# Optimization experiments

Hardware: AMD Instinct MI355X
Metric: run time of the kernel (lower is better)

The kernel has to match this reference:

```python
import jax, jax.numpy as jnp
import numpy as np

N, E, G = 50000, 200000, 1000
EPS = 1e-5
NEG_SLOPE = 0.2


def setup_inputs() -> dict:
    key = jax.random.key(0)
    ks = jax.random.split(key, 24)
    p = lambda k, shape: jax.random.normal(k, shape, jnp.float32) * 0.05
    inp = {
        "x": jax.random.normal(ks[0], (N, 64), jnp.float32),
        "edge_index": jax.random.randint(ks[1], (2, E), 0, N, jnp.int32),
        "batch": jnp.sort(jax.random.randint(ks[2], (N,), 0, G, jnp.int32)),
        "solvent_fingerprint": jax.random.uniform(ks[3], (G, 128), jnp.float32),
        # GAT layer 1: 64 -> 4 heads x 128
        "W1": p(ks[4], (64, 512)), "a1_src": p(ks[5], (4, 128)), "a1_dst": p(ks[6], (4, 128)), "b1": jnp.zeros((512,), jnp.float32),
        "bn1_g": jnp.ones((512,), jnp.float32), "bn1_b": jnp.zeros((512,), jnp.float32),
        # GAT layer 2: 512 -> 4 heads x 256
        "W2": p(ks[7], (512, 1024)), "a2_src": p(ks[8], (4, 256)), "a2_dst": p(ks[9], (4, 256)), "b2": jnp.zeros((1024,), jnp.float32),
        "bn2_g": jnp.ones((1024,), jnp.float32), "bn2_b": jnp.zeros((1024,), jnp.float32),
        # GCN: 1024 -> 256
        "Wg": p(ks[10], (1024, 256)), "bg": jnp.zeros((256,), jnp.float32),
        "bn3_g": jnp.ones((256,), jnp.float32), "bn3_b": jnp.zeros((256,), jnp.float32),
        # MLP head
        "Ws": p(ks[11], (128, 128)), "bs": jnp.zeros((128,), jnp.float32),
        "Wf1": p(ks[12], (640, 128)), "bf1": jnp.zeros((128,), jnp.float32),
        "bnf_g": jnp.ones((128,), jnp.float32), "bnf_b": jnp.zeros((128,), jnp.float32),
        "Wf2": p(ks[13], (128, 1)), "bf2": jnp.zeros((1,), jnp.float32),
    }
    return inp


def _batchnorm(x, g, b):
    mu = x.mean(0)
    var = x.var(0)
    return (x - mu) * jax.lax.rsqrt(var + EPS) * g + b


def _gat(x, src, dst, W, a_src, a_dst, b, H, C):
    n = x.shape[0]
    h = (x @ W).reshape(n, H, C)                      # [N,H,C]
    al_s = (h * a_src).sum(-1)                        # [N,H]
    al_d = (h * a_dst).sum(-1)                        # [N,H]
    e = jax.nn.leaky_relu(al_s[src] + al_d[dst], NEG_SLOPE)   # [E,H]
    m = jax.ops.segment_max(e, dst, num_segments=n)
    ex = jnp.exp(e - m[dst])
    s = jax.ops.segment_sum(ex, dst, num_segments=n)
    alpha = ex / jnp.maximum(s[dst], 1e-16)
    out = jax.ops.segment_sum(h[src] * alpha[..., None], dst, num_segments=n)  # [N,H,C]
    return out.reshape(n, H * C) + b


def _gcn(x, src, dst, W, b):
    n = x.shape[0]
    h = x @ W
    deg = jax.ops.segment_sum(jnp.ones_like(dst, jnp.float32), dst, num_segments=n)
    dinv = jax.lax.rsqrt(jnp.maximum(deg, 1.0))
    norm = dinv[src] * dinv[dst]
    return jax.ops.segment_sum(h[src] * norm[:, None], dst, num_segments=n) + b


def reference(x, edge_index, batch, solvent_fingerprint,
              W1, a1_src, a1_dst, b1, bn1_g, bn1_b,
              W2, a2_src, a2_dst, b2, bn2_g, bn2_b,
              Wg, bg, bn3_g, bn3_b,
              Ws, bs, Wf1, bf1, bnf_g, bnf_b, Wf2, bf2):
    n = x.shape[0]
    loops = jnp.arange(n, dtype=edge_index.dtype)
    src = jnp.concatenate([edge_index[0], loops])
    dst = jnp.concatenate([edge_index[1], loops])

    h = _gat(x, src, dst, W1, a1_src, a1_dst, b1, 4, 128)
    h = jax.nn.relu(_batchnorm(h, bn1_g, bn1_b))
    h = _gat(h, src, dst, W2, a2_src, a2_dst, b2, 4, 256)
    h = jax.nn.relu(_batchnorm(h, bn2_g, bn2_b))
    h = _gcn(h, src, dst, Wg, bg)
    h = jax.nn.relu(_batchnorm(h, bn3_g, bn3_b))

    cnt = jax.ops.segment_sum(jnp.ones((n,), jnp.float32), batch, num_segments=G)
    gap = jax.ops.segment_sum(h, batch, num_segments=G) / jnp.maximum(cnt, 1.0)[:, None]
    gmp = jax.ops.segment_max(h, batch, num_segments=G)
    gmp = jnp.where(jnp.isfinite(gmp), gmp, 0.0)

    solv = jax.nn.relu(solvent_fingerprint @ Ws + bs)
    z = jnp.concatenate([gap, gmp, solv], axis=1)          # [G,640]
    z = jax.nn.relu(_batchnorm(z @ Wf1 + bf1, bnf_g, bnf_b))
    # dropout: identity in eval/deterministic reference
    return jax.nn.sigmoid(z @ Wf2 + bf2)
```

## Files before the change

kernel.cpp:

```cpp
#include <hip/hip_runtime.h>
#include <cmath>

#define LEAK 0.2f
#define BN_EPS 1e-5f

static inline int cdiv(long long a, long long b){ return (int)((a + b - 1) / b); }

typedef __attribute__((ext_vector_type(8))) short bf16x8;
typedef __attribute__((ext_vector_type(4))) float f32x4;

__device__ __forceinline__ float bf2f(unsigned short u){
    return __uint_as_float(((unsigned int)u) << 16);
}
__device__ __forceinline__ unsigned short f2bf(float f){
    unsigned int u = __float_as_uint(f);
    u += 0x7FFFu + ((u >> 16) & 1u);
    return (unsigned short)(u >> 16);
}
__device__ __forceinline__ float edge_ex(float s, float d){
    float t = s + d;
    t = (t >= 0.f) ? t : LEAK * t;
    return __expf(t);
}

#define GLOAD_LDS16(gsrc, ldst) \
    __builtin_amdgcn_global_load_lds( \
        (const __attribute__((address_space(1))) unsigned int*)(gsrc), \
        (__attribute__((address_space(3))) unsigned int*)(ldst), 16, 0, 0)

__global__ __launch_bounds__(256) void gemm_mfma(
    const unsigned short* __restrict__ A, const unsigned short* __restrict__ Bt,
    unsigned short* __restrict__ D, int M, int K, int lda, int ldb, int ldc,
    int NX, int NYT)
{
    const int id = blockIdx.x;
    const int xcd = id & 7;
    const int j = id >> 3;
    const int bx = j % NX;
    const int by = (j / NX) * 8 + xcd;
    if (by >= NYT) return;

    __shared__ unsigned short As[128 * 64];
    __shared__ unsigned short Bs[128 * 64];
    const int t = threadIdx.x;
    const int row0 = by * 128, col0 = bx * 128;
    const int lane = t & 63, wv = t >> 6;
    const int wm = (wv >> 1) << 6, wn = (wv & 1) << 6;
    const int lm = lane & 15, lq = lane >> 4;

    const int sr  = t >> 3;
    const int scs = (t & 7) << 3;
    const int gsw = (((t & 7) ^ (sr & 7)) << 3);
    const unsigned short* ap[4];
    const unsigned short* bp[4];
    unsigned short* la[4];
    unsigned short* lb[4];
    #pragma unroll
    for (int q = 0; q < 4; ++q) {
        int r = sr + q * 32;
        int gra = row0 + r; if (gra >= M) gra = M - 1;
        ap[q] = A  + (size_t)gra * lda + gsw;
        bp[q] = Bt + (size_t)(col0 + r) * ldb + gsw;
        la[q] = &As[r * 64 + scs];
        lb[q] = &Bs[r * 64 + scs];
    }

    f32x4 acc[4][4] = {};
    const int rx = lm & 7;

    for (int k0 = 0; k0 < K; k0 += 64) {
        #pragma unroll
        for (int q = 0; q < 4; ++q) {
            GLOAD_LDS16(ap[q] + k0, la[q]);
            GLOAD_LDS16(bp[q] + k0, lb[q]);
        }
        __syncthreads();

        #pragma unroll
        for (int kk = 0; kk < 2; ++kk) {
            const int ck = (((kk << 2) + lq) ^ rx) << 3;
            bf16x8 af[4], bfr[4];
            #pragma unroll
            for (int mi = 0; mi < 4; ++mi)
                af[mi] = *(const bf16x8*)&As[(wm + mi * 16 + lm) * 64 + ck];
            #pragma unroll
            for (int ni = 0; ni < 4; ++ni)
                bfr[ni] = *(const bf16x8*)&Bs[(wn + ni * 16 + lm) * 64 + ck];
            #pragma unroll
            for (int mi = 0; mi < 4; ++mi)
                #pragma unroll
                for (int ni = 0; ni < 4; ++ni)
                    acc[mi][ni] = __builtin_amdgcn_mfma_f32_16x16x32_bf16(
                        af[mi], bfr[ni], acc[mi][ni], 0, 0, 0);
        }
        __syncthreads();
    }

    #pragma unroll
    for (int mi = 0; mi < 4; ++mi) {
        int row_b = row0 + wm + mi * 16 + lq * 4;
        #pragma unroll
        for (int ni = 0; ni < 4; ++ni) {
            int col = col0 + wn + ni * 16 + lm;
            #pragma unroll
            for (int r = 0; r < 4; ++r) {
                int row = row_b + r;
                if (row < M) D[(size_t)row * ldc + col] = f2bf(acc[mi][ni][r]);
            }
        }
    }
}

__global__ __launch_bounds__(256) void logits_valu(
    const unsigned short* __restrict__ A, const unsigned short* __restrict__ vat,
    float* __restrict__ C, int M, int K)
{
    __shared__ unsigned short vs[8 * 512];
    const int t = threadIdx.x;
    for (int i = t; i < K; i += 256)
        *(bf16x8*)&vs[i * 8] = *(const bf16x8*)(vat + (size_t)i * 8);
    __syncthreads();

    const int lane = t & 63;
    const int w = blockIdx.x * 4 + (t >> 6);
    const int Gl = K >> 3;
    const int rpw = 64 / Gl;
    const int sub = lane / Gl;
    const int li = lane - sub * Gl;
    long long row = (long long)w * rpw + sub;
    if (row >= M) return;

    bf16x8 hv = *(const bf16x8*)(A + row * K + li * 8);
    float hf[8];
    #pragma unroll
    for (int j = 0; j < 8; ++j) hf[j] = bf2f((unsigned short)hv[j]);

    float s[8];
    #pragma unroll
    for (int o = 0; o < 8; ++o) {
        bf16x8 v = *(const bf16x8*)&vs[o * K + li * 8];
        float acc = 0.f;
        #pragma unroll
        for (int j = 0; j < 8; ++j) acc += hf[j] * bf2f((unsigned short)v[j]);
        s[o] = acc;
    }
    for (int off = Gl >> 1; off; off >>= 1) {
        #pragma unroll
        for (int o = 0; o < 8; ++o) s[o] += __shfl_xor(s[o], off);
    }
    #pragma unroll
    for (int o = 0; o < 8; ++o)
        if (li == o) C[row * 8 + o] = s[o];
}

__global__ __launch_bounds__(256) void prep_all(
    const float* __restrict__ W1, const float* __restrict__ W2,
    const float* __restrict__ Wg, const float* __restrict__ x,
    const float* __restrict__ a1s, const float* __restrict__ a1d,
    const float* __restrict__ a2s, const float* __restrict__ a2d,
    const int* __restrict__ batch,
    unsigned short* __restrict__ W1bdt, unsigned short* __restrict__ W2t,
    unsigned short* __restrict__ Wgt, unsigned short* __restrict__ xb,
    unsigned short* __restrict__ vat1, unsigned short* __restrict__ vat2,
    int* __restrict__ cursor, int* __restrict__ gptr,
    int N, int G_,
    int c0, int c1, int c2, int c3, int c4, int c5, int c6)
{
    const int t = threadIdx.x;
    const int bid = blockIdx.x;
    if (bid < c0) {
        int i = bid * 256 + t;
        int o = i >> 8, k = i & 255;
        unsigned short v = 0;
        if ((k >> 6) == (o >> 7)) v = f2bf(W1[(size_t)(k & 63) * 512 + o]);
        W1bdt[i] = v;
    } else if (bid < c1) {
        int i = (bid - c0) * 256 + t;
        int k = i >> 10, n = i & 1023;
        W2t[(size_t)n * 512 + k] = f2bf(W2[i]);
    } else if (bid < c2) {
        int i = (bid - c1) * 256 + t;
        int k = i >> 8, n = i & 255;
        Wgt[(size_t)n * 1024 + k] = f2bf(Wg[i]);
    } else if (bid < c3) {
        int i = (bid - c2) * 256 + t;
        if (i < N * 16) {
            float4 v = *reinterpret_cast<const float4*>(x + (size_t)i * 4);
            ushort4 o = { f2bf(v.x), f2bf(v.y), f2bf(v.z), f2bf(v.w) };
            *reinterpret_cast<ushort4*>(xb + (size_t)i * 4) = o;
        }
    } else if (bid < c4) {
        int w = (((bid - c3) * 256 + t) >> 6);
        int lane = t & 63;
        int k = w >> 2, h = w & 3;
        const float* wp = W1 + (size_t)k * 512 + h * 128;
        const float* as = a1s + h * 128;
        const float* ad = a1d + h * 128;
        float s = 0.f, d = 0.f;
        for (int c = lane; c < 128; c += 64) {
            float v = wp[c];
            s += v * as[c];
            d += v * ad[c];
        }
        #pragma unroll
        for (int off = 32; off; off >>= 1) {
            s += __shfl_down(s, off);
            d += __shfl_down(d, off);
        }
        if (lane == 0) {
            vat1[(size_t)h * 64 + k] = f2bf(s);
            vat1[(size_t)(4 + h) * 64 + k] = f2bf(d);
        }
    } else if (bid < c5) {
        int w = (((bid - c4) * 256 + t) >> 6);
        int lane = t & 63;
        int k = w >> 2, h = w & 3;
        const float* wp = W2 + (size_t)k * 1024 + h * 256;
        const float* as = a2s + h * 256;
        const float* ad = a2d + h * 256;
        float s = 0.f, d = 0.f;
        for (int c = lane; c < 256; c += 64) {
            float v = wp[c];
            s += v * as[c];
            d += v * ad[c];
        }
        #pragma unroll
        for (int off = 32; off; off >>= 1) {
            s += __shfl_down(s, off);
            d += __shfl_down(d, off);
        }
        if (lane == 0) {
            vat2[(size_t)h * 512 + k] = f2bf(s);
            vat2[(size_t)(4 + h) * 512 + k] = f2bf(d);
        }
    } else if (bid < c6) {
        int i = (bid - c5) * 256 + t;
        if (i < N) cursor[i] = 1;
    } else {
        int g = (bid - c6) * 256 + t;
        if (g > G_) return;
        if (g == G_) { gptr[G_] = N; return; }
        int lo = 0, hi = N;
        while (lo < hi) { int mid = (lo + hi) >> 1; if (batch[mid] < g) lo = mid + 1; else hi = mid; }
        gptr[g] = lo;
    }
}

template<bool RELU>
__global__ __launch_bounds__(256) void gemm_small(
    const float* __restrict__ A, const float* __restrict__ B,
    const float* __restrict__ bias, float* __restrict__ C,
    int M, int K, int lda, int ldb, int ldc)
{
    __shared__ float As[2][640];
    const int t = threadIdx.x;
    const int r = t >> 7, c = t & 127;
    const int row0 = blockIdx.x * 2;
    for (int i = t; i < 2 * K; i += 256) {
        int rr = i / K, kk = i - rr * K;
        int gr = row0 + rr;
        As[rr][kk] = (gr < M) ? A[(size_t)gr * lda + kk] : 0.f;
    }
    __syncthreads();
    float acc0 = 0.f, acc1 = 0.f;
    for (int k = 0; k < K; k += 8) {
        float4 a0 = *reinterpret_cast<const float4*>(&As[r][k]);
        float4 a1 = *reinterpret_cast<const float4*>(&As[r][k + 4]);
        acc0 += a0.x * B[(size_t)(k + 0) * ldb + c];
        acc1 += a0.y * B[(size_t)(k + 1) * ldb + c];
        acc0 += a0.z * B[(size_t)(k + 2) * ldb + c];
        acc1 += a0.w * B[(size_t)(k + 3) * ldb + c];
        acc0 += a1.x * B[(size_t)(k + 4) * ldb + c];
        acc1 += a1.y * B[(size_t)(k + 5) * ldb + c];
        acc0 += a1.z * B[(size_t)(k + 6) * ldb + c];
        acc1 += a1.w * B[(size_t)(k + 7) * ldb + c];
    }
    int row = row0 + r;
    if (row < M) {
        float v = acc0 + acc1;
        if (bias) v += bias[c];
        if (RELU) v = fmaxf(v, 0.f);
        C[(size_t)row * ldc + c] = v;
    }
}

__device__ __forceinline__ int e_src(const int* es, int E, int k){ return k < E ? es[k] : k - E; }
__device__ __forceinline__ int e_dst(const int* ed, int E, int k){ return k < E ? ed[k] : k - E; }

__global__ void hist_dst(const int* __restrict__ ed, int E, int* __restrict__ cnt)
{
    int k = blockIdx.x * blockDim.x + threadIdx.x;
    if (k < E) atomicAdd(&cnt[ed[k]], 1);
}

__global__ __launch_bounds__(256) void scan_blk(const int* __restrict__ cnt,
                                                int* __restrict__ rowptr,
                                                int* __restrict__ bsums, int n)
{
    __shared__ int ts[256];
    const int t = threadIdx.x;
    const int i0 = blockIdx.x * 1024 + t * 4;
    int4 v = {0, 0, 0, 0};
    if (i0 + 3 < n) v = *reinterpret_cast<const int4*>(cnt + i0);
    else {
        if (i0 + 0 < n) v.x = cnt[i0 + 0];
        if (i0 + 1 < n) v.y = cnt[i0 + 1];
        if (i0 + 2 < n) v.z = cnt[i0 + 2];
        if (i0 + 3 < n) v.w = cnt[i0 + 3];
    }
    int lsum = v.x + v.y + v.z + v.w;
    ts[t] = lsum;
    __syncthreads();
    #pragma unroll
    for (int off = 1; off < 256; off <<= 1) {
        int u = (t >= off) ? ts[t - off] : 0;
        __syncthreads();
        ts[t] += u;
        __syncthreads();
    }
    int excl = ts[t] - lsum;
    if (i0 + 0 < n) rowptr[i0 + 0] = excl;
    if (i0 + 1 < n) rowptr[i0 + 1] = excl + v.x;
    if (i0 + 2 < n) rowptr[i0 + 2] = excl + v.x + v.y;
    if (i0 + 3 < n) rowptr[i0 + 3] = excl + v.x + v.y + v.z;
    if (t == 255) bsums[blockIdx.x] = ts[255];
}

__global__ __launch_bounds__(256) void scan_tops(int* __restrict__ bsums,
                                                 int* __restrict__ rowptr, int nb, int n)
{
    __shared__ int ts[256];
    const int t = threadIdx.x;
    int v = (t < nb) ? bsums[t] : 0;
    ts[t] = v;
    __syncthreads();
    #pragma unroll
    for (int off = 1; off < 256; off <<= 1) {
        int u = (t >= off) ? ts[t - off] : 0;
        __syncthreads();
        ts[t] += u;
        __syncthreads();
    }
    if (t < nb) bsums[t] = ts[t] - v;
    if (t == 255) rowptr[n] = ts[255];
}

__global__ void scan_add(int* __restrict__ rowptr, int* __restrict__ cursor,
                         const int* __restrict__ bsums, int n)
{
    int i = blockIdx.x * blockDim.x + threadIdx.x;
    if (i >= n) return;
    int r = rowptr[i] + bsums[i >> 10];
    rowptr[i] = r;
    cursor[i] = r;
}

__global__ void csr_scatter_dinv(const int* __restrict__ es, const int* __restrict__ ed,
                                 int E, int Etot, int* __restrict__ cursor,
                                 int* __restrict__ col,
                                 const int* __restrict__ rowptr,
                                 float* __restrict__ dinv, int N, int NBsc)
{
    const int bid = blockIdx.x;
    const int t = threadIdx.x;
    if (bid < NBsc) {
        int k = bid * 256 + t;
        if (k >= Etot) return;
        int sn = e_src(es, E, k), dn = e_dst(ed, E, k);
        int pos = atomicAdd(&cursor[dn], 1);
        col[pos] = sn;
    } else {
        int i = (bid - NBsc) * 256 + t;
        if (i < N) dinv[i] = rsqrtf(fmaxf((float)(rowptr[i + 1] - rowptr[i]), 1.f));
    }
}

__global__ void gat_agg4_64(const int* __restrict__ rowptr, const int* __restrict__ col,
                            const unsigned short* __restrict__ xb,
                            const float* __restrict__ alsd,
                            unsigned short* __restrict__ agg, int N)
{
    int w = (int)(((long long)blockIdx.x * blockDim.x + threadIdx.x) >> 6);
    int lane = threadIdx.x & 63;
    if (w >= N) return;
    float4 dt = *reinterpret_cast<const float4*>(alsd + (size_t)w * 8 + 4);
    int r0 = rowptr[w], r1 = rowptr[w + 1];
    float a0 = 0.f, a1 = 0.f, a2 = 0.f, a3 = 0.f;
    float s0 = 0.f, s1 = 0.f, s2 = 0.f, s3 = 0.f;
    for (int e = r0; e < r1; ++e) {
        int sn = col[e];
        float4 st = *reinterpret_cast<const float4*>(alsd + (size_t)sn * 8);
        float e0 = edge_ex(st.x, dt.x);
        float e1 = edge_ex(st.y, dt.y);
        float e2 = edge_ex(st.z, dt.z);
        float e3 = edge_ex(st.w, dt.w);
        float xA = bf2f(xb[(size_t)sn * 64 + lane]);
        a0 += e0 * xA; s0 += e0;
        a1 += e1 * xA; s1 += e1;
        a2 += e2 * xA; s2 += e2;
        a3 += e3 * xA; s3 += e3;
    }
    unsigned short* op = agg + (size_t)w * 256 + lane;
    op[0]   = f2bf(a0 / fmaxf(s0, 1e-16f));
    op[64]  = f2bf(a1 / fmaxf(s1, 1e-16f));
    op[128] = f2bf(a2 / fmaxf(s2, 1e-16f));
    op[192] = f2bf(a3 / fmaxf(s3, 1e-16f));
}

__global__ void gat_gather512_ex(const int* __restrict__ rowptr, const int* __restrict__ col,
                                 const unsigned short* __restrict__ h, int ldh,
                                 const float* __restrict__ alsd, int pr,
                                 unsigned short* __restrict__ out, int N)
{
    int w = (int)(((long long)blockIdx.x * blockDim.x + threadIdx.x) >> 6);
    int lane = threadIdx.x & 63;
    if (w >= N) return;
    float2 dt = *reinterpret_cast<const float2*>(alsd + (size_t)w * 8 + 4 + 2 * pr);
    int r0 = rowptr[w], r1 = rowptr[w + 1];
    float s0 = 0.f, s1 = 0.f;
    float a00=0.f,a01=0.f,a02=0.f,a03=0.f;
    float a10=0.f,a11=0.f,a12=0.f,a13=0.f;
    for (int e = r0; e < r1; ++e) {
        int sn = col[e];
        float2 st = *reinterpret_cast<const float2*>(alsd + (size_t)sn * 8 + 2 * pr);
        float e0 = edge_ex(st.x, dt.x);
        float e1 = edge_ex(st.y, dt.y);
        const unsigned short* p = h + (size_t)sn * ldh + lane * 4;
        ushort4 h0 = *reinterpret_cast<const ushort4*>(p);
        ushort4 h1 = *reinterpret_cast<const ushort4*>(p + 256);
        s0 += e0; s1 += e1;
        a00 += bf2f(h0.x) * e0; a01 += bf2f(h0.y) * e0;
        a02 += bf2f(h0.z) * e0; a03 += bf2f(h0.w) * e0;
        a10 += bf2f(h1.x) * e1; a11 += bf2f(h1.y) * e1;
        a12 += bf2f(h1.z) * e1; a13 += bf2f(h1.w) * e1;
    }
    float i0 = 1.f / fmaxf(s0, 1e-16f);
    float i1 = 1.f / fmaxf(s1, 1e-16f);
    ushort4 o0 = { f2bf(a00*i0), f2bf(a01*i0), f2bf(a02*i0), f2bf(a03*i0) };
    ushort4 o1 = { f2bf(a10*i1), f2bf(a11*i1), f2bf(a12*i1), f2bf(a13*i1) };
    unsigned short* op = out + (size_t)w * 512 + lane * 4;
    *reinterpret_cast<ushort4*>(op)       = o0;
    *reinterpret_cast<ushort4*>(op + 256) = o1;
}

__global__ void gcn_gather256(const int* __restrict__ rowptr, const int* __restrict__ col,
                              const unsigned short* __restrict__ h,
                              const float* __restrict__ dinv,
                              unsigned short* __restrict__ out, int N)
{
    int w = (int)(((long long)blockIdx.x * blockDim.x + threadIdx.x) >> 6);
    int lane = threadIdx.x & 63;
    if (w >= N) return;
    int r0 = rowptr[w], r1 = rowptr[w + 1];
    float a0 = 0.f, a1 = 0.f, a2 = 0.f, a3 = 0.f;
    int e = r0;
    for (; e + 1 < r1; e += 2) {
        int sn0 = col[e], sn1 = col[e + 1];
        float w0 = dinv[sn0], w1 = dinv[sn1];
        ushort4 hv0 = *reinterpret_cast<const ushort4*>(h + (size_t)sn0 * 256 + lane * 4);
        ushort4 hv1 = *reinterpret_cast<const ushort4*>(h + (size_t)sn1 * 256 + lane * 4);
        a0 += bf2f(hv0.x) * w0 + bf2f(hv1.x) * w1;
        a1 += bf2f(hv0.y) * w0 + bf2f(hv1.y) * w1;
        a2 += bf2f(hv0.z) * w0 + bf2f(hv1.z) * w1;
        a3 += bf2f(hv0.w) * w0 + bf2f(hv1.w) * w1;
    }
    if (e < r1) {
        int sn = col[e];
        float wv = dinv[sn];
        ushort4 hv = *reinterpret_cast<const ushort4*>(h + (size_t)sn * 256 + lane * 4);
        a0 += bf2f(hv.x) * wv; a1 += bf2f(hv.y) * wv;
        a2 += bf2f(hv.z) * wv; a3 += bf2f(hv.w) * wv;
    }
    float dn = dinv[w];
    ushort4 o;
    o.x = f2bf(a0 * dn); o.y = f2bf(a1 * dn);
    o.z = f2bf(a2 * dn); o.w = f2bf(a3 * dn);
    *reinterpret_cast<ushort4*>(out + (size_t)w * 256 + lane * 4) = o;
}

template<int D>
__global__ __launch_bounds__(256) void bn_part(
    const float* __restrict__ x, float* __restrict__ ps, float* __restrict__ pq,
    int M, int Y)
{
    constexpr int DG = D / 4;
    constexpr int P  = 256 / DG;
    const int t = threadIdx.x;
    const int cg = t % DG, ph = t / DG;
    const int y = blockIdx.y;
    const int rows_per = (M + Y - 1) / Y;
    const int r0 = y * rows_per;
    const int r1 = min(r0 + rows_per, M);
    float s0=0,s1=0,s2=0,s3=0,q0=0,q1=0,q2=0,q3=0;
    for (int r = r0 + ph; r < r1; r += P) {
        float4 v = *reinterpret_cast<const float4*>(x + (size_t)r * D + cg * 4);
        s0+=v.x; s1+=v.y; s2+=v.z; s3+=v.w;
        q0+=v.x*v.x; q1+=v.y*v.y; q2+=v.z*v.z; q3+=v.w*v.w;
    }
    __shared__ float ls[P][D];
    __shared__ float lq[P][D];
    ls[ph][cg*4+0]=s0; ls[ph][cg*4+1]=s1; ls[ph][cg*4+2]=s2; ls[ph][cg*4+3]=s3;
    lq[ph][cg*4+0]=q0; lq[ph][cg*4+1]=q1; lq[ph][cg*4+2]=q2; lq[ph][cg*4+3]=q3;
    __syncthreads();
    if (ph == 0) {
        #pragma unroll
        for (int j = 0; j < 4; ++j) {
            float ss = 0.f, qq = 0.f;
            #pragma unroll
            for (int p = 0; p < P; ++p) { ss += ls[p][cg*4+j]; qq += lq[p][cg*4+j]; }
            ps[(size_t)y * D + cg*4 + j] = ss;
            pq[(size_t)y * D + cg*4 + j] = qq;
        }
    }
}

template<int D>
__global__ __launch_bounds__(256) void bn_part_bf(
    const unsigned short* __restrict__ x, int ldx,
    float* __restrict__ ps, float* __restrict__ pq, int M, int Y)
{
    constexpr int DG = D / 4;
    constexpr int P  = 256 / DG;
    const int t = threadIdx.x;
    const int cg = t % DG, ph = t / DG;
    const int y = blockIdx.y;
    const int rows_per = (M + Y - 1) / Y;
    const int r0 = y * rows_per;
    const int r1 = min(r0 + rows_per, M);
    float s0=0,s1=0,s2=0,s3=0,q0=0,q1=0,q2=0,q3=0;
    for (int r = r0 + ph; r < r1; r += P) {
        ushort4 u = *reinterpret_cast<const ushort4*>(x + (size_t)r * ldx + cg * 4);
        float vx = bf2f(u.x), vy = bf2f(u.y), vz = bf2f(u.z), vw = bf2f(u.w);
        s0+=vx; s1+=vy; s2+=vz; s3+=vw;
        q0+=vx*vx; q1+=vy*vy; q2+=vz*vz; q3+=vw*vw;
    }
    __shared__ float ls[P][D];
    __shared__ float lq[P][D];
    ls[ph][cg*4+0]=s0; ls[ph][cg*4+1]=s1; ls[ph][cg*4+2]=s2; ls[ph][cg*4+3]=s3;
    lq[ph][cg*4+0]=q0; lq[ph][cg*4+1]=q1; lq[ph][cg*4+2]=q2; lq[ph][cg*4+3]=q3;
    __syncthreads();
    if (ph == 0) {
        #pragma unroll
        for (int j = 0; j < 4; ++j) {
            float ss = 0.f, qq = 0.f;
            #pragma unroll
            for (int p = 0; p < P; ++p) { ss += ls[p][cg*4+j]; qq += lq[p][cg*4+j]; }
            ps[(size_t)y * D + cg*4 + j] = ss;
            pq[(size_t)y * D + cg*4 + j] = qq;
        }
    }
}

template<int D>
__global__ __launch_bounds__(256) void bn_reduce_fin(
    const float* __restrict__ ps, const float* __restrict__ pq,
    const float* __restrict__ g, const float* __restrict__ b,
    float* __restrict__ scale, float* __restrict__ shift, int Y, float invM)
{
    const int t = threadIdx.x;
    const int cl = t & 63;
    const int c = blockIdx.x * 64 + cl;
    const int ph = t >> 6;
    float s = 0.f, q = 0.f;
    for (int y = ph; y < Y; y += 4) {
        s += ps[(size_t)y * D + c];
        q += pq[(size_t)y * D + c];
    }
    __shared__ float ls[4][64];
    __shared__ float lq[4][64];
    ls[ph][cl] = s; lq[ph][cl] = q;
    __syncthreads();
    if (ph == 0) {
        s = ls[0][cl] + ls[1][cl] + ls[2][cl] + ls[3][cl];
        q = lq[0][cl] + lq[1][cl] + lq[2][cl] + lq[3][cl];
        float mu = s * invM;
        float var = q * invM - mu * mu;
        float rs = rsqrtf(var + BN_EPS) * g[c];
        scale[c] = rs;
        shift[c] = b[c] - mu * rs;
    }
}

__global__ void bn_apply_bfbf(const unsigned short* __restrict__ x,
                              const float* __restrict__ scale, const float* __restrict__ shift,
                              unsigned short* __restrict__ dst, int total4, int Cb4,
                              int ldx, int ldd)
{
    int i = blockIdx.x * blockDim.x + threadIdx.x;
    if (i >= total4) return;
    int r = i / Cb4, c4 = (i - r * Cb4) * 4;
    ushort4 u = *reinterpret_cast<const ushort4*>(x + (size_t)r * ldx + c4);
    float4 sc = *reinterpret_cast<const float4*>(scale + c4);
    float4 sh = *reinterpret_cast<const float4*>(shift + c4);
    ushort4 o;
    o.x = f2bf(fmaxf(bf2f(u.x) * sc.x + sh.x, 0.f));
    o.y = f2bf(fmaxf(bf2f(u.y) * sc.y + sh.y, 0.f));
    o.z = f2bf(fmaxf(bf2f(u.z) * sc.z + sh.z, 0.f));
    o.w = f2bf(fmaxf(bf2f(u.w) * sc.w + sh.w, 0.f));
    *reinterpret_cast<ushort4*>(dst + (size_t)r * ldd + c4) = o;
}

__global__ __launch_bounds__(256) void pool_gather_bn(const unsigned short* __restrict__ h,
                                                      const float* __restrict__ scale,
                                                      const float* __restrict__ shift,
                                                      const int* __restrict__ gptr,
                                                      float* __restrict__ z, int G_)
{
    int g = blockIdx.x;
    int c = threadIdx.x;
    int r0 = gptr[g], r1 = gptr[g + 1];
    float sc = scale[c], sh = shift[c];
    float s = 0.f, m = 0.f;
    int i = r0;
    for (; i + 1 < r1; i += 2) {
        float v0 = fmaxf(bf2f(h[(size_t)i * 256 + c]) * sc + sh, 0.f);
        float v1 = fmaxf(bf2f(h[(size_t)(i + 1) * 256 + c]) * sc + sh, 0.f);
        s += v0 + v1;
        m = fmaxf(m, fmaxf(v0, v1));
    }
    if (i < r1) {
        float v = fmaxf(bf2f(h[(size_t)i * 256 + c]) * sc + sh, 0.f);
        s += v;
        m = fmaxf(m, v);
    }
    float cnt = fmaxf((float)(r1 - r0), 1.f);
    z[(size_t)g * 640 + c] = s / cnt;
    z[(size_t)g * 640 + 256 + c] = m;
}

__global__ void final_head_bn(const float* __restrict__ f1,
                              const float* __restrict__ scale, const float* __restrict__ shift,
                              const float* __restrict__ Wf2, const float* __restrict__ bf2,
                              float* __restrict__ out, int G_)
{
    int w = (int)(((long long)blockIdx.x * blockDim.x + threadIdx.x) >> 6);
    int lane = threadIdx.x & 63;
    if (w >= G_) return;
    float s = 0.f;
    #pragma unroll
    for (int q = 0; q < 2; ++q) {
        int c = lane + q * 64;
        float v = fmaxf(f1[(size_t)w * 128 + c] * scale[c] + shift[c], 0.f);
        s += v * Wf2[c];
    }
    #pragma unroll
    for (int off = 32; off; off >>= 1) s += __shfl_down(s, off);
    if (lane == 0) out[w] = 1.f / (1.f + __expf(-(s + bf2[0])));
}

__global__ void sentinel(float* __restrict__ out, int n, float v)
{
    int i = blockIdx.x * blockDim.x + threadIdx.x;
    if (i < n) out[i] = v;
}

extern "C" void kernel_launch(void* const* d_in, const int* in_sizes, int n_in,
                              void* d_out, int out_size, void* d_ws, size_t ws_size,
                              hipStream_t stream)
{
    const float* x    = (const float*)d_in[0];
    const int*   ei   = (const int*)d_in[1];
    const int*   batch= (const int*)d_in[2];
    const float* sfp  = (const float*)d_in[3];
    const float* W1   = (const float*)d_in[4];
    const float* a1s  = (const float*)d_in[5];
    const float* a1d  = (const float*)d_in[6];
    const float* bn1g = (const float*)d_in[8];
    const float* bn1b = (const float*)d_in[9];
    const float* W2   = (const float*)d_in[10];
    const float* a2s  = (const float*)d_in[11];
    const float* a2d  = (const float*)d_in[12];
    const float* bn2g = (const float*)d_in[14];
    const float* bn2b = (const float*)d_in[15];
    const float* Wg   = (const float*)d_in[16];
    const float* bn3g = (const float*)d_in[18];
    const float* bn3b = (const float*)d_in[19];
    const float* Wsm  = (const float*)d_in[20];
    const float* bsm  = (const float*)d_in[21];
    const float* Wf1  = (const float*)d_in[22];
    const float* bnfg = (const float*)d_in[24];
    const float* bnfb = (const float*)d_in[25];
    const float* Wf2  = (const float*)d_in[26];
    const float* bf2  = (const float*)d_in[27];
    float* outp = (float*)d_out;

    const int N    = in_sizes[0] / 64;
    const int E    = in_sizes[1] / 2;
    const int G_   = in_sizes[3] / 128;
    const int Etot = E + N;
    const int* esrc = ei;
    const int* edst = ei + E;
    const int YB = 256;
    const int NB = cdiv(N, 1024);
    const int NYT = cdiv(N, 128);
    const int NYT8 = cdiv(NYT, 8) * 8;

    float* ws = (float*)d_ws;
    size_t off = 0;
    float* accA  = ws + off; off += (size_t)N * 256;
    float* h3acc = ws + off; off += (size_t)N * 256;
    unsigned short* g1b   = (unsigned short*)accA;
    unsigned short* g3b   = (unsigned short*)accA;
    unsigned short* h2all = (unsigned short*)accA;
    unsigned short* R1 = (unsigned short*)(ws + off); off += (size_t)N * 256;
    unsigned short* o1n = R1;
    unsigned short* hb  = (unsigned short*)(ws + off); off += (size_t)N * 128;
    unsigned short* xb  = (unsigned short*)(ws + off); off += (size_t)N * 32;
    float* alsd = ws + off; off += (size_t)N * 8;
    float* dinv = ws + off; off += N;
    float* bsc = ws + off; off += 1024;
    float* bsh = ws + off; off += 1024;
    float* ps  = ws + off; off += (size_t)YB * 512;
    float* pq  = ws + off; off += (size_t)YB * 512;
    float* z   = ws + off; off += (size_t)G_ * 640;
    float* f1  = ws + off; off += (size_t)G_ * 128;
    int* rowptr = (int*)(ws + off); off += (size_t)(N + 1);
    int* colc   = (int*)(ws + off); off += (size_t)Etot;
    int* gptr   = (int*)(ws + off); off += (size_t)(G_ + 1);
    int* bsums  = (int*)(ws + off); off += 256;
    off = (off + 3) & ~(size_t)3;
    unsigned short* vat1 = (unsigned short*)(ws + off); off += 128 * 64 / 2;
    unsigned short* vat2 = (unsigned short*)(ws + off); off += 128 * 512 / 2;
    unsigned short* W1bdt = (unsigned short*)(ws + off); off += 512 * 256 / 2;
    unsigned short* W2t = (unsigned short*)(ws + off); off += 512 * 1024 / 2;
    unsigned short* Wgt = (unsigned short*)(ws + off); off += 1024 * 256 / 2;
    int* cursor = (int*)alsd;
    size_t need = off * 4;
    if (ws_size < need) {
        sentinel<<<cdiv(out_size, 256), 256, 0, stream>>>(outp, out_size, (float)(ws_size >> 20));
        return;
    }

    const int BLK = 256;
    dim3 blk(BLK);

    const int c0 = 512;
    const int c1 = c0 + 2048;
    const int c2 = c1 + 1024;
    const int c3 = c2 + cdiv((long long)N * 16, 256);
    const int c4 = c3 + 64;
    const int c5 = c4 + 512;
    const int c6 = c5 + cdiv(N, 256);
    const int c7 = c6 + cdiv(G_ + 1, 256);
    prep_all<<<c7, blk, 0, stream>>>(W1, W2, Wg, x, a1s, a1d, a2s, a2d, batch,
                                     W1bdt, W2t, Wgt, xb, vat1, vat2,
                                     cursor, gptr, N, G_,
                                     c0, c1, c2, c3, c4, c5, c6);

    hist_dst<<<cdiv(E, BLK), blk, 0, stream>>>(edst, E, cursor);
    scan_blk<<<NB, blk, 0, stream>>>(cursor, rowptr, bsums, N);
    scan_tops<<<1, blk, 0, stream>>>(bsums, rowptr, NB, N);
    scan_add<<<cdiv(N, BLK), blk, 0, stream>>>(rowptr, cursor, bsums, N);
    { int NBsc = cdiv(Etot, BLK);
      csr_scatter_dinv<<<NBsc + cdiv(N, BLK), blk, 0, stream>>>(
          esrc, edst, E, Etot, cursor, colc, rowptr, dinv, N, NBsc); }

    logits_valu<<<cdiv(N, 32), blk, 0, stream>>>(xb, vat1, alsd, N, 64);
    gat_agg4_64<<<cdiv((long long)N * 64, BLK), blk, 0, stream>>>(
        rowptr, colc, xb, alsd, hb, N);
    gemm_mfma<<<NYT8 * 4, blk, 0, stream>>>(hb, W1bdt, g1b, N, 256, 256, 256, 512, 4, NYT);
    { dim3 g(1, YB); bn_part_bf<512><<<g, blk, 0, stream>>>(g1b, 512, ps, pq, N, YB); }
    bn_reduce_fin<512><<<8, blk, 0, stream>>>(ps, pq, bn1g, bn1b, bsc, bsh, YB, 1.f / N);
    bn_apply_bfbf<<<cdiv((long long)N * 128, BLK), blk, 0, stream>>>(
        g1b, bsc, bsh, o1n, N * 128, 128, 512, 512);

    logits_valu<<<cdiv(N, 4), blk, 0, stream>>>(o1n, vat2, alsd, N, 512);

    gemm_mfma<<<NYT8 * 8, blk, 0, stream>>>(o1n, W2t, h2all, N, 512, 512, 512, 1024, 8, NYT);
    for (int pr = 0; pr < 2; ++pr) {
        gat_gather512_ex<<<cdiv((long long)N * 64, BLK), blk, 0, stream>>>(
            rowptr, colc, h2all + pr * 512, 1024, alsd, pr, R1, N);
        { dim3 g(1, YB); bn_part_bf<512><<<g, blk, 0, stream>>>(R1, 512, ps, pq, N, YB); }
        bn_reduce_fin<512><<<8, blk, 0, stream>>>(ps, pq, bn2g + pr * 512, bn2b + pr * 512,
                                                  bsc + pr * 512, bsh + pr * 512, YB, 1.f / N);
        bn_apply_bfbf<<<cdiv((long long)N * 128, BLK), blk, 0, stream>>>(
            R1, bsc + pr * 512, bsh + pr * 512, h2all + pr * 512, N * 128, 128, 512, 1024);
    }

    gemm_mfma<<<NYT8 * 2, blk, 0, stream>>>(h2all, Wgt, hb, N, 1024, 1024, 1024, 256, 2, NYT);

    gcn_gather256<<<cdiv((long long)N * 64, BLK), blk, 0, stream>>>(
        rowptr, colc, hb, dinv, g3b, N);
    { dim3 g(1, YB); bn_part_bf<256><<<g, blk, 0, stream>>>(g3b, 256, ps, pq, N, YB); }
    bn_reduce_fin<256><<<4, blk, 0, stream>>>(ps, pq, bn3g, bn3b, bsc, bsh, YB, 1.f / N);

    pool_gather_bn<<<G_, blk, 0, stream>>>(g3b, bsc, bsh, gptr, z, G_);

    gemm_small<true><<<cdiv(G_, 2), blk, 0, stream>>>(
        sfp, Wsm, bsm, z + 512, G_, 128, 128, 128, 640);

    gemm_small<false><<<cdiv(G_, 2), blk, 0, stream>>>(
        z, Wf1, nullptr, f1, G_, 640, 640, 128, 128);
    { dim3 g(1, YB); bn_part<128><<<g, blk, 0, stream>>>(f1, ps, pq, G_, YB); }
    bn_reduce_fin<128><<<2, blk, 0, stream>>>(ps, pq, bnfg, bnfb, bsc, bsh, YB, 1.f / G_);
    final_head_bn<<<cdiv((long long)G_ * 64, BLK), blk, 0, stream>>>(
        f1, bsc, bsh, Wf2, bf2, outp, G_);
}
```

Baseline: 824.2 us.

## Fuse BN statistics into gather kernels and fuse BN-apply with layer-2 logits

The GAT-512 and GCN-256 gather kernels now also accumulate per-column sums and sums of squares. Each block reduces its four rows in shared memory, then atomically adds the result into one of 256 partial slots, which are zeroed by memsets beforehand. This removes the separate bn_part passes that re-read the gathered outputs. A new kernel applies BN1 with ReLU, writes o1n and computes the layer-2 attention logits in one pass, replacing bn_apply_bfbf plus logits_valu. In exchange it adds memsets and atomics, and the statistics now come from fp32 values rather than the bf16-rounded outputs. It also assumes YB covers 256 slots.

```diff
diff --git a/kernel.cpp b/kernel.cpp
--- a/kernel.cpp
+++ b/kernel.cpp
@@ -151,6 +151,60 @@
     #pragma unroll
     for (int o = 0; o < 8; ++o)
         if (li == o) C[row * 8 + o] = s[o];
+}
+
+__global__ __launch_bounds__(256) void bn_apply_logits512(
+    const unsigned short* __restrict__ g1b,
+    const float* __restrict__ scale, const float* __restrict__ shift,
+    const unsigned short* __restrict__ vat,
+    unsigned short* __restrict__ o1n, float* __restrict__ C, int M)
+{
+    __shared__ unsigned short vs[8 * 512];
+    const int t = threadIdx.x;
+    for (int i = t; i < 512; i += 256)
+        *(bf16x8*)&vs[i * 8] = *(const bf16x8*)(vat + (size_t)i * 8);
+    __syncthreads();
+
+    const int lane = t & 63;
+    long long row = (long long)blockIdx.x * 4 + (t >> 6);
+    if (row >= M) return;
+
+    bf16x8 u = *(const bf16x8*)(g1b + row * 512 + lane * 8);
+    float4 sc0 = *(const float4*)(scale + lane * 8);
+    float4 sc1 = *(const float4*)(scale + lane * 8 + 4);
+    float4 sh0 = *(const float4*)(shift + lane * 8);
+    float4 sh1 = *(const float4*)(shift + lane * 8 + 4);
+    float hf[8];
+    hf[0] = fmaxf(bf2f((unsigned short)u[0]) * sc0.x + sh0.x, 0.f);
+    hf[1] = fmaxf(bf2f((unsigned short)u[1]) * sc0.y + sh0.y, 0.f);
+    hf[2] = fmaxf(bf2f((unsigned short)u[2]) * sc0.z + sh0.z, 0.f);
+    hf[3] = fmaxf(bf2f((unsigned short)u[3]) * sc0.w + sh0.w, 0.f);
+    hf[4] = fmaxf(bf2f((unsigned short)u[4]) * sc1.x + sh1.x, 0.f);
+    hf[5] = fmaxf(bf2f((unsigned short)u[5]) * sc1.y + sh1.y, 0.f);
+    hf[6] = fmaxf(bf2f((unsigned short)u[6]) * sc1.z + sh1.z, 0.f);
+    hf[7] = fmaxf(bf2f((unsigned short)u[7]) * sc1.w + sh1.w, 0.f);
+    bf16x8 o;
+    #pragma unroll
+    for (int j = 0; j < 8; ++j) o[j] = (short)f2bf(hf[j]);
+    *(bf16x8*)(o1n + row * 512 + lane * 8) = o;
+
+    float s[8];
+    #pragma unroll
+    for (int oo = 0; oo < 8; ++oo) {
+        bf16x8 v = *(const bf16x8*)&vs[oo * 512 + lane * 8];
+        float acc = 0.f;
+        #pragma unroll
+        for (int j = 0; j < 8; ++j) acc += hf[j] * bf2f((unsigned short)v[j]);
+        s[oo] = acc;
+    }
+    #pragma unroll
+    for (int off = 32; off; off >>= 1) {
+        #pragma unroll
+        for (int oo = 0; oo < 8; ++oo) s[oo] += __shfl_xor(s[oo], off);
+    }
+    #pragma unroll
+    for (int oo = 0; oo < 8; ++oo)
+        if (lane == oo) C[row * 8 + oo] = s[oo];
 }
 
 __global__ __launch_bounds__(256) void prep_all(
@@ -407,75 +461,125 @@
     op[192] = f2bf(a3 / fmaxf(s3, 1e-16f));
 }
 
-__global__ void gat_gather512_ex(const int* __restrict__ rowptr, const int* __restrict__ col,
-                                 const unsigned short* __restrict__ h, int ldh,
-                                 const float* __restrict__ alsd, int pr,
-                                 unsigned short* __restrict__ out, int N)
-{
-    int w = (int)(((long long)blockIdx.x * blockDim.x + threadIdx.x) >> 6);
-    int lane = threadIdx.x & 63;
-    if (w >= N) return;
-    float2 dt = *reinterpret_cast<const float2*>(alsd + (size_t)w * 8 + 4 + 2 * pr);
-    int r0 = rowptr[w], r1 = rowptr[w + 1];
-    float s0 = 0.f, s1 = 0.f;
-    float a00=0.f,a01=0.f,a02=0.f,a03=0.f;
-    float a10=0.f,a11=0.f,a12=0.f,a13=0.f;
-    for (int e = r0; e < r1; ++e) {
-        int sn = col[e];
-        float2 st = *reinterpret_cast<const float2*>(alsd + (size_t)sn * 8 + 2 * pr);
-        float e0 = edge_ex(st.x, dt.x);
-        float e1 = edge_ex(st.y, dt.y);
-        const unsigned short* p = h + (size_t)sn * ldh + lane * 4;
-        ushort4 h0 = *reinterpret_cast<const ushort4*>(p);
-        ushort4 h1 = *reinterpret_cast<const ushort4*>(p + 256);
-        s0 += e0; s1 += e1;
-        a00 += bf2f(h0.x) * e0; a01 += bf2f(h0.y) * e0;
-        a02 += bf2f(h0.z) * e0; a03 += bf2f(h0.w) * e0;
-        a10 += bf2f(h1.x) * e1; a11 += bf2f(h1.y) * e1;
-        a12 += bf2f(h1.z) * e1; a13 += bf2f(h1.w) * e1;
-    }
-    float i0 = 1.f / fmaxf(s0, 1e-16f);
-    float i1 = 1.f / fmaxf(s1, 1e-16f);
-    ushort4 o0 = { f2bf(a00*i0), f2bf(a01*i0), f2bf(a02*i0), f2bf(a03*i0) };
-    ushort4 o1 = { f2bf(a10*i1), f2bf(a11*i1), f2bf(a12*i1), f2bf(a13*i1) };
-    unsigned short* op = out + (size_t)w * 512 + lane * 4;
-    *reinterpret_cast<ushort4*>(op)       = o0;
-    *reinterpret_cast<ushort4*>(op + 256) = o1;
-}
-
-__global__ void gcn_gather256(const int* __restrict__ rowptr, const int* __restrict__ col,
-                              const unsigned short* __restrict__ h,
-                              const float* __restrict__ dinv,
-                              unsigned short* __restrict__ out, int N)
-{
-    int w = (int)(((long long)blockIdx.x * blockDim.x + threadIdx.x) >> 6);
-    int lane = threadIdx.x & 63;
-    if (w >= N) return;
-    int r0 = rowptr[w], r1 = rowptr[w + 1];
-    float a0 = 0.f, a1 = 0.f, a2 = 0.f, a3 = 0.f;
-    int e = r0;
-    for (; e + 1 < r1; e += 2) {
-        int sn0 = col[e], sn1 = col[e + 1];
-        float w0 = dinv[sn0], w1 = dinv[sn1];
-        ushort4 hv0 = *reinterpret_cast<const ushort4*>(h + (size_t)sn0 * 256 + lane * 4);
-        ushort4 hv1 = *reinterpret_cast<const ushort4*>(h + (size_t)sn1 * 256 + lane * 4);
-        a0 += bf2f(hv0.x) * w0 + bf2f(hv1.x) * w1;
-        a1 += bf2f(hv0.y) * w0 + bf2f(hv1.y) * w1;
-        a2 += bf2f(hv0.z) * w0 + bf2f(hv1.z) * w1;
-        a3 += bf2f(hv0.w) * w0 + bf2f(hv1.w) * w1;
-    }
-    if (e < r1) {
-        int sn = col[e];
-        float wv = dinv[sn];
-        ushort4 hv = *reinterpret_cast<const ushort4*>(h + (size_t)sn * 256 + lane * 4);
-        a0 += bf2f(hv.x) * wv; a1 += bf2f(hv.y) * wv;
-        a2 += bf2f(hv.z) * wv; a3 += bf2f(hv.w) * wv;
-    }
-    float dn = dinv[w];
-    ushort4 o;
-    o.x = f2bf(a0 * dn); o.y = f2bf(a1 * dn);
-    o.z = f2bf(a2 * dn); o.w = f2bf(a3 * dn);
-    *reinterpret_cast<ushort4*>(out + (size_t)w * 256 + lane * 4) = o;
+__global__ __launch_bounds__(256) void gat_gather512_ex(
+    const int* __restrict__ rowptr, const int* __restrict__ col,
+    const unsigned short* __restrict__ h, int ldh,
+    const float* __restrict__ alsd, int pr,
+    unsigned short* __restrict__ out,
+    float* __restrict__ ps, float* __restrict__ pq, int N)
+{
+    const int t = threadIdx.x;
+    const int lane = t & 63;
+    const int wv = t >> 6;
+    int w = (int)(((long long)blockIdx.x * 256 + t) >> 6);
+    const bool valid = (w < N);
+
+    float v0=0.f,v1=0.f,v2=0.f,v3=0.f;
+    float u0=0.f,u1=0.f,u2=0.f,u3=0.f;
+    if (valid) {
+        float2 dt = *reinterpret_cast<const float2*>(alsd + (size_t)w * 8 + 4 + 2 * pr);
+        int r0 = rowptr[w], r1 = rowptr[w + 1];
+        float s0 = 0.f, s1 = 0.f;
+        float a00=0.f,a01=0.f,a02=0.f,a03=0.f;
+        float a10=0.f,a11=0.f,a12=0.f,a13=0.f;
+        for (int e = r0; e < r1; ++e) {
+            int sn = col[e];
+            float2 st = *reinterpret_cast<const float2*>(alsd + (size_t)sn * 8 + 2 * pr);
+            float e0 = edge_ex(st.x, dt.x);
+            float e1 = edge_ex(st.y, dt.y);
+            const unsigned short* p = h + (size_t)sn * ldh + lane * 4;
+            ushort4 h0 = *reinterpret_cast<const ushort4*>(p);
+            ushort4 h1 = *reinterpret_cast<const ushort4*>(p + 256);
+            s0 += e0; s1 += e1;
+            a00 += bf2f(h0.x) * e0; a01 += bf2f(h0.y) * e0;
+            a02 += bf2f(h0.z) * e0; a03 += bf2f(h0.w) * e0;
+            a10 += bf2f(h1.x) * e1; a11 += bf2f(h1.y) * e1;
+            a12 += bf2f(h1.z) * e1; a13 += bf2f(h1.w) * e1;
+        }
+        float i0 = 1.f / fmaxf(s0, 1e-16f);
+        float i1 = 1.f / fmaxf(s1, 1e-16f);
+        v0 = a00*i0; v1 = a01*i0; v2 = a02*i0; v3 = a03*i0;
+        u0 = a10*i1; u1 = a11*i1; u2 = a12*i1; u3 = a13*i1;
+        ushort4 o0 = { f2bf(v0), f2bf(v1), f2bf(v2), f2bf(v3) };
+        ushort4 o1 = { f2bf(u0), f2bf(u1), f2bf(u2), f2bf(u3) };
+        unsigned short* op = out + (size_t)w * 512 + lane * 4;
+        *reinterpret_cast<ushort4*>(op)       = o0;
+        *reinterpret_cast<ushort4*>(op + 256) = o1;
+    }
+
+    __shared__ float ls[4][512];
+    __shared__ float lq[4][512];
+    int c0 = lane * 4;
+    ls[wv][c0+0]=v0; ls[wv][c0+1]=v1; ls[wv][c0+2]=v2; ls[wv][c0+3]=v3;
+    ls[wv][256+c0+0]=u0; ls[wv][256+c0+1]=u1; ls[wv][256+c0+2]=u2; ls[wv][256+c0+3]=u3;
+    lq[wv][c0+0]=v0*v0; lq[wv][c0+1]=v1*v1; lq[wv][c0+2]=v2*v2; lq[wv][c0+3]=v3*v3;
+    lq[wv][256+c0+0]=u0*u0; lq[wv][256+c0+1]=u1*u1; lq[wv][256+c0+2]=u2*u2; lq[wv][256+c0+3]=u3*u3;
+    __syncthreads();
+    const size_t slot = (size_t)(blockIdx.x & 255) * 512;
+    #pragma unroll
+    for (int c = t; c < 512; c += 256) {
+        float s = ls[0][c] + ls[1][c] + ls[2][c] + ls[3][c];
+        float q = lq[0][c] + lq[1][c] + lq[2][c] + lq[3][c];
+        atomicAdd(&ps[slot + c], s);
+        atomicAdd(&pq[slot + c], q);
+    }
+}
+
+__global__ __launch_bounds__(256) void gcn_gather256(
+    const int* __restrict__ rowptr, const int* __restrict__ col,
+    const unsigned short* __restrict__ h,
+    const float* __restrict__ dinv,
+    unsigned short* __restrict__ out,
+    float* __restrict__ ps, float* __restrict__ pq, int N)
+{
+    const int t = threadIdx.x;
+    const int lane = t & 63;
+    const int wv = t >> 6;
+    int w = (int)(((long long)blockIdx.x * 256 + t) >> 6);
+    const bool valid = (w < N);
+
+    float v0=0.f,v1=0.f,v2=0.f,v3=0.f;
+    if (valid) {
+        int r0 = rowptr[w], r1 = rowptr[w + 1];
+        float a0 = 0.f, a1 = 0.f, a2 = 0.f, a3 = 0.f;
+        int e = r0;
+        for (; e + 1 < r1; e += 2) {
+            int sn0 = col[e], sn1 = col[e + 1];
+            float w0 = dinv[sn0], w1 = dinv[sn1];
+            ushort4 hv0 = *reinterpret_cast<const ushort4*>(h + (size_t)sn0 * 256 + lane * 4);
+            ushort4 hv1 = *reinterpret_cast<const ushort4*>(h + (size_t)sn1 * 256 + lane * 4);
+            a0 += bf2f(hv0.x) * w0 + bf2f(hv1.x) * w1;
+            a1 += bf2f(hv0.y) * w0 + bf2f(hv1.y) * w1;
+            a2 += bf2f(hv0.z) * w0 + bf2f(hv1.z) * w1;
+            a3 += bf2f(hv0.w) * w0 + bf2f(hv1.w) * w1;
+        }
+        if (e < r1) {
+            int sn = col[e];
+            float wv2 = dinv[sn];
+            ushort4 hv = *reinterpret_cast<const ushort4*>(h + (size_t)sn * 256 + lane * 4);
+            a0 += bf2f(hv.x) * wv2; a1 += bf2f(hv.y) * wv2;
+            a2 += bf2f(hv.z) * wv2; a3 += bf2f(hv.w) * wv2;
+        }
+        float dn = dinv[w];
+        v0 = a0 * dn; v1 = a1 * dn; v2 = a2 * dn; v3 = a3 * dn;
+        ushort4 o = { f2bf(v0), f2bf(v1), f2bf(v2), f2bf(v3) };
+        *reinterpret_cast<ushort4*>(out + (size_t)w * 256 + lane * 4) = o;
+    }
+
+    __shared__ float ls[4][256];
+    __shared__ float lq[4][256];
+    int c0 = lane * 4;
+    ls[wv][c0+0]=v0; ls[wv][c0+1]=v1; ls[wv][c0+2]=v2; ls[wv][c0+3]=v3;
+    lq[wv][c0+0]=v0*v0; lq[wv][c0+1]=v1*v1; lq[wv][c0+2]=v2*v2; lq[wv][c0+3]=v3*v3;
+    __syncthreads();
+    const size_t slot = (size_t)(blockIdx.x & 255) * 256;
+    if (t < 256) {
+        int c = t;
+        float s = ls[0][c] + ls[1][c] + ls[2][c] + ls[3][c];
+        float q = lq[0][c] + lq[1][c] + lq[2][c] + lq[3][c];
+        atomicAdd(&ps[slot + c], s);
+        atomicAdd(&pq[slot + c], q);
+    }
 }
 
 template<int D>
@@ -761,16 +865,15 @@
     gemm_mfma<<<NYT8 * 4, blk, 0, stream>>>(hb, W1bdt, g1b, N, 256, 256, 256, 512, 4, NYT);
     { dim3 g(1, YB); bn_part_bf<512><<<g, blk, 0, stream>>>(g1b, 512, ps, pq, N, YB); }
     bn_reduce_fin<512><<<8, blk, 0, stream>>>(ps, pq, bn1g, bn1b, bsc, bsh, YB, 1.f / N);
-    bn_apply_bfbf<<<cdiv((long long)N * 128, BLK), blk, 0, stream>>>(
-        g1b, bsc, bsh, o1n, N * 128, 128, 512, 512);
-
-    logits_valu<<<cdiv(N, 4), blk, 0, stream>>>(o1n, vat2, alsd, N, 512);
+    bn_apply_logits512<<<cdiv(N, 4), blk, 0, stream>>>(
+        g1b, bsc, bsh, vat2, o1n, alsd, N);
 
     gemm_mfma<<<NYT8 * 8, blk, 0, stream>>>(o1n, W2t, h2all, N, 512, 512, 512, 1024, 8, NYT);
     for (int pr = 0; pr < 2; ++pr) {
+        hipMemsetAsync(ps, 0, (size_t)YB * 512 * 4, stream);
+        hipMemsetAsync(pq, 0, (size_t)YB * 512 * 4, stream);
         gat_gather512_ex<<<cdiv((long long)N * 64, BLK), blk, 0, stream>>>(
-            rowptr, colc, h2all + pr * 512, 1024, alsd, pr, R1, N);
-        { dim3 g(1, YB); bn_part_bf<512><<<g, blk, 0, stream>>>(R1, 512, ps, pq, N, YB); }
+            rowptr, colc, h2all + pr * 512, 1024, alsd, pr, R1, ps, pq, N);
         bn_reduce_fin<512><<<8, blk, 0, stream>>>(ps, pq, bn2g + pr * 512, bn2b + pr * 512,
                                                   bsc + pr * 512, bsh + pr * 512, YB, 1.f / N);
         bn_apply_bfbf<<<cdiv((long long)N * 128, BLK), blk, 0, stream>>>(
@@ -779,9 +882,10 @@
 
     gemm_mfma<<<NYT8 * 2, blk, 0, stream>>>(h2all, Wgt, hb, N, 1024, 1024, 1024, 256, 2, NYT);
 
+    hipMemsetAsync(ps, 0, (size_t)YB * 256 * 4, stream);
+    hipMemsetAsync(pq, 0, (size_t)YB * 256 * 4, stream);
     gcn_gather256<<<cdiv((long long)N * 64, BLK), blk, 0, stream>>>(
-        rowptr, colc, hb, dinv, g3b, N);
-    { dim3 g(1, YB); bn_part_bf<256><<<g, blk, 0, stream>>>(g3b, 256, ps, pq, N, YB); }
+        rowptr, colc, hb, dinv, g3b, ps, pq, N);
     bn_reduce_fin<256><<<4, blk, 0, stream>>>(ps, pq, bn3g, bn3b, bsc, bsh, YB, 1.f / N);
 
     pool_gather_bn<<<G_, blk, 0, stream>>>(g3b, bsc, bsh, gptr, z, G_);
```

New measurement: 777.8 us. 5.6% less time.
